# Performance work log

Measured on AMD Instinct MI355X. Metric: run time of the kernel, lower is better.

Reference implementation:

```python
import jax, jax.numpy as jnp
import numpy as np

# dims per module source / chosen globals
B, LB = 4, 28            # new frames, buffered frames; M = B+LB = L = 32
DK, DV = 256, 32         # Dk=256 hardcoded; Dv = 4*len_of_lookup+4 with len_of_lookup=7
HS, WS = 64, 64          # H//8, W//8 with H=W=512
LMAX = 32                # memory cap L
TRAIN_SZ = 1000          # log base train_sz
ALPHA = 0.5              # blend coefficient (original inits 0, which zeroes the branch)
# log(L*h*w + h*w, train_sz) / sqrt(Dk)
SCALE = float(np.log(LMAX * HS * WS + HS * WS) / np.log(TRAIN_SZ) / np.sqrt(DK))


def _xavier(key, fan_in, fan_out):
    lim = np.sqrt(6.0 / (fan_in + fan_out))
    return jax.random.uniform(key, (fan_in, fan_out), jnp.float32, -lim, lim)


def setup_inputs() -> dict:
    key = jax.random.key(0)
    ks = jax.random.split(key, 7)
    return {
        "fc": jax.random.normal(ks[0], (B, DK, HS, WS), jnp.float32),
        "fm": jax.random.normal(ks[1], (B, DV, HS, WS), jnp.float32),
        "key_buffer": jax.random.normal(ks[2], (LB, DK, HS, WS), jnp.float32),
        "value_buffer": jax.random.normal(ks[3], (LB, DV, HS, WS), jnp.float32),
        "Q": _xavier(ks[4], DK, DK),
        "K": _xavier(ks[5], DK, DK),
        "V": _xavier(ks[6], DV, DV),
    }


def reference(fc, fm, key_buffer, value_buffer, Q, K, V):
    # matmul = einsum('ijkl,jm->imkl'): per-pixel channel mixing
    q = jnp.einsum('bdhw,de->behw', fc, Q)                      # [B,Dk,h,w]
    k = jnp.concatenate([jnp.einsum('bdhw,de->behw', fc, K), key_buffer], axis=0)    # [M,Dk,h,w]
    v = jnp.concatenate([jnp.einsum('bdhw,de->behw', fm, V), value_buffer], axis=0)  # [M,Dv,h,w]
    # current_batch (=1) < L, so no slicing of k/v on this step
    scores = SCALE * jnp.einsum('bdhw,mdhw->bmhw', q, k)        # [B,M,h,w]
    attn = jax.nn.softmax(scores, axis=-1)                      # NOTE: softmax over width axis, as in source (dim=-1)
    ctx = jnp.einsum('bmhw,mdhw->bdhw', attn, v)                # [B,Dv,h,w]
    return fm + ALPHA * ctx
```

## Files before the change

kernel.cpp:

```cpp
#include <hip/hip_runtime.h>
#include <hip/hip_bf16.h>
#include <cmath>

#define NB 4
#define NM 32
#define DKc 256
#define DVc 32
#define NP 4096

using bf16x8 = __attribute__((ext_vector_type(8))) short;
using f32x4  = __attribute__((ext_vector_type(4))) float;

__device__ __forceinline__ unsigned short f2bf(float f) {
    union { float f; unsigned u; } x; x.f = f;
    unsigned r = 0x7FFFu + ((x.u >> 16) & 1u);
    return (unsigned short)((x.u + r) >> 16);
}

__global__ __launch_bounds__(256) void k_prep(
    const float* __restrict__ fc, unsigned short* __restrict__ fcT,
    const float* __restrict__ Q, unsigned short* __restrict__ WTq,
    const float* __restrict__ K, unsigned short* __restrict__ WTk,
    const float* __restrict__ fm, const float* __restrict__ V, float* __restrict__ vproj) {
    int x = blockIdx.x;
    int t = threadIdx.x;
    if (x < 1056) {
        __shared__ float tile[64][65];
        const float* s; unsigned short* d; int R, C, r0, c0;
        if (x < 1024) {
            int bb = x >> 8, rest = x & 255;
            R = 256; C = 4096;
            r0 = (rest >> 6) * 64; c0 = (rest & 63) * 64;
            s = fc + (long)bb * 256 * 4096; d = fcT + (long)bb * 256 * 4096;
        } else {
            int i = x - 1024;
            int mat = i >> 4, idx = i & 15;
            R = 256; C = 256;
            r0 = (idx >> 2) * 64; c0 = (idx & 3) * 64;
            s = mat ? K : Q; d = mat ? WTk : WTq;
        }
        #pragma unroll
        for (int j = 0; j < 16; ++j) {
            int i = t + 256 * j;
            int r = i >> 6, c = i & 63;
            tile[r][c] = s[(long)(r0 + r) * C + c0 + c];
        }
        __syncthreads();
        #pragma unroll
        for (int j = 0; j < 8; ++j) {
            int i = t + 256 * j;
            int row = i >> 5;
            int pr = i & 31;
            float f0 = tile[2 * pr][row];
            float f1 = tile[2 * pr + 1][row];
            unsigned pack = (unsigned)f2bf(f0) | ((unsigned)f2bf(f1) << 16);
            reinterpret_cast<unsigned*>(d)[(((long)(c0 + row) * R + r0) >> 1) + pr] = pack;
        }
    } else {
        __shared__ float Vl[32][32];
        __shared__ float fml[32][256];
        int i = x - 1056;
        int b = i >> 4, p0 = (i & 15) * 256;
        #pragma unroll
        for (int j = 0; j < 4; ++j) { int ii = t + 256 * j; Vl[ii >> 5][ii & 31] = V[ii]; }
        for (int j = 0; j < 32; ++j) {
            int ii = t + 256 * j;
            int dd = ii >> 8, c = ii & 255;
            fml[dd][c] = fm[((long)b * DVc + dd) * NP + p0 + c];
        }
        __syncthreads();
        float acc[32];
        #pragma unroll
        for (int e = 0; e < 32; ++e) acc[e] = 0.f;
        for (int dd = 0; dd < 32; ++dd) {
            float fv = fml[dd][t];
            #pragma unroll
            for (int e = 0; e < 32; ++e) acc[e] += fv * Vl[dd][e];
        }
        #pragma unroll
        for (int e = 0; e < 32; ++e) vproj[((long)b * DVc + e) * NP + p0 + t] = acc[e];
    }
}

__global__ __launch_bounds__(256) void k_proj(
    const unsigned short* __restrict__ WTq, const unsigned short* __restrict__ WTk,
    const unsigned short* __restrict__ fcT,
    float* __restrict__ qproj, float* __restrict__ kproj) {
    int t = threadIdx.x;
    int wave = t >> 6, lane = t & 63;
    int y = blockIdx.y;
    int b = y & 3, mat = y >> 2;
    int p0 = blockIdx.x * 64;
    int ln = lane & 15, quad = lane >> 4;
    const unsigned short* WT = mat ? WTk : WTq;
    float* dst = mat ? kproj : qproj;
    int e0w = wave * 64;
    const unsigned short* bbase = fcT + ((long)b * NP + p0 + ln) * DKc + quad * 8;
    f32x4 acc[4][4] = {};
    for (int kk = 0; kk < DKc; kk += 32) {
        bf16x8 a[4], bb[4];
        #pragma unroll
        for (int i = 0; i < 4; ++i)
            a[i] = *reinterpret_cast<const bf16x8*>(WT + (long)(e0w + i * 16 + ln) * DKc + quad * 8 + kk);
        #pragma unroll
        for (int j = 0; j < 4; ++j)
            bb[j] = *reinterpret_cast<const bf16x8*>(bbase + (long)j * 16 * DKc + kk);
        #pragma unroll
        for (int i = 0; i < 4; ++i)
            #pragma unroll
            for (int j = 0; j < 4; ++j)
                acc[i][j] = __builtin_amdgcn_mfma_f32_16x16x32_bf16(a[i], bb[j], acc[i][j], 0, 0, 0);
    }
    #pragma unroll
    for (int i = 0; i < 4; ++i)
        #pragma unroll
        for (int j = 0; j < 4; ++j)
            #pragma unroll
            for (int r = 0; r < 4; ++r) {
                int e = e0w + i * 16 + quad * 4 + r, p = p0 + j * 16 + ln;
                dst[((long)b * DKc + e) * NP + p] = acc[i][j][r];
            }
}

__global__ __launch_bounds__(256, 2) void k_scores(
    const float* __restrict__ qproj, const float* __restrict__ kproj,
    const float* __restrict__ kbuf, float* __restrict__ partial) {
    int t = threadIdx.x;
    int wseg = blockIdx.x, ec = blockIdx.y, b = blockIdx.z;
    int w = wseg * 256 + t;
    int e0 = ec * 32;
    const float* qp = qproj + ((long)b * DKc + e0) * NP + w;
    float acc[NM];
    #pragma unroll
    for (int m = 0; m < NM; ++m) acc[m] = 0.f;
    #pragma unroll 2
    for (int e = 0; e < 32; ++e) {
        float qv = qp[(long)e * NP];
        float kv[NM];
        #pragma unroll
        for (int m = 0; m < NM; ++m) {
            const float* kp = (m < 4 ? kproj + (long)m * DKc * NP
                                     : kbuf + (long)(m - 4) * DKc * NP);
            kv[m] = kp[(long)(e0 + e) * NP + w];
        }
        #pragma unroll
        for (int m = 0; m < NM; ++m) acc[m] += qv * kv[m];
    }
    float* pp = partial + (((long)b * 8 + ec) * NM) * NP + w;
    #pragma unroll
    for (int m = 0; m < NM; ++m) pp[(long)m * NP] = acc[m];
}

__global__ __launch_bounds__(512) void k_out(
    const float* __restrict__ partial, const float* __restrict__ vproj,
    const float* __restrict__ vbuf, const float* __restrict__ fm,
    float* __restrict__ out, float scale) {
    __shared__ float sc[32][68];
    int t = threadIdx.x;
    int b = blockIdx.x >> 6, hrow = blockIdx.x & 63;
    int p0h = hrow * 64;
    int wave = t >> 6, lane = t & 63;
    {
        int w = t & 63, mg = t >> 6;
        float s[4] = {0.f, 0.f, 0.f, 0.f};
        #pragma unroll
        for (int c = 0; c < 8; ++c) {
            const float* pp = partial + (((long)b * 8 + c) * NM + mg * 4) * NP + p0h + w;
            #pragma unroll
            for (int mi = 0; mi < 4; ++mi) s[mi] += pp[(long)mi * NP];
        }
        #pragma unroll
        for (int mi = 0; mi < 4; ++mi) sc[mg * 4 + mi][w] = s[mi] * scale;
    }
    __syncthreads();
    #pragma unroll
    for (int r = 0; r < 4; ++r) {
        int m = wave * 4 + r;
        float x = sc[m][lane];
        float mx = x;
        #pragma unroll
        for (int d = 1; d < 64; d <<= 1) mx = fmaxf(mx, __shfl_xor(mx, d));
        float e = __expf(x - mx);
        float sum = e;
        #pragma unroll
        for (int d = 1; d < 64; d <<= 1) sum += __shfl_xor(sum, d);
        sc[m][lane] = e / sum;
    }
    __syncthreads();
    {
        int dg = t >> 6, w = t & 63;
        float c4[4] = {0.f, 0.f, 0.f, 0.f};
        #pragma unroll
        for (int m = 0; m < NM; ++m) {
            float a = sc[m][w];
            const float* vp = (m < 4 ? vproj + (long)m * DVc * NP : vbuf + (long)(m - 4) * DVc * NP)
                              + (long)(dg * 4) * NP + p0h + w;
            #pragma unroll
            for (int i = 0; i < 4; ++i) c4[i] += a * vp[(long)i * NP];
        }
        #pragma unroll
        for (int i = 0; i < 4; ++i) {
            long gi = ((long)b * DVc + dg * 4 + i) * NP + p0h + w;
            out[gi] = fm[gi] + 0.5f * c4[i];
        }
    }
}

extern "C" void kernel_launch(void* const* d_in, const int* in_sizes, int n_in,
                              void* d_out, int out_size, void* d_ws, size_t ws_size,
                              hipStream_t stream) {
    const float* fc = (const float*)d_in[0];
    const float* fm = (const float*)d_in[1];
    const float* kb = (const float*)d_in[2];
    const float* vb = (const float*)d_in[3];
    const float* Q  = (const float*)d_in[4];
    const float* K  = (const float*)d_in[5];
    const float* V  = (const float*)d_in[6];
    float* out = (float*)d_out;
    char* ws = (char*)d_ws;
    float*          qproj = (float*)(ws);
    float*          kproj = (float*)(ws + 16777216);
    float*          vproj = (float*)(ws + 33554432);
    unsigned short* fcT   = (unsigned short*)(ws + 35651584);
    unsigned short* WTq   = (unsigned short*)(ws + 44040192);
    unsigned short* WTk   = (unsigned short*)(ws + 44171264);
    float*          partial = (float*)(ws + 35651584);
    float scale = (float)(log(135168.0) / log(1000.0) / 16.0);

    hipLaunchKernelGGL(k_prep, dim3(1120), dim3(256), 0, stream,
                       fc, fcT, Q, WTq, K, WTk, fm, V, vproj);
    hipLaunchKernelGGL(k_proj, dim3(64, 8), dim3(256), 0, stream,
                       WTq, WTk, fcT, qproj, kproj);
    hipLaunchKernelGGL(k_scores, dim3(16, 8, 4), dim3(256), 0, stream,
                       qproj, kproj, kb, partial);
    hipLaunchKernelGGL(k_out, dim3(256), dim3(512), 0, stream,
                       partial, vproj, vb, fm, out, scale);
}
```

Before: 266.9 us.

## Retile score kernel over batch and key groups to reuse key loads

The score kernel is reorganised so each block computes all four query batches against a group of four memory keys, instead of one batch against all 32 keys. Each key slice is now read from global memory once rather than once per batch, while query slices are re-read once per key group. Loads and stores also move to two-wide float vectors per thread. The grid changes to 8x8x8 blocks. The trade-off is more query traffic and a different register footprint per thread.

```diff
diff --git a/kernel.cpp b/kernel.cpp
--- a/kernel.cpp
+++ b/kernel.cpp
@@ -10,6 +10,7 @@
 
 using bf16x8 = __attribute__((ext_vector_type(8))) short;
 using f32x4  = __attribute__((ext_vector_type(4))) float;
+using f32x2  = __attribute__((ext_vector_type(2))) float;
 
 __device__ __forceinline__ unsigned short f2bf(float f) {
     union { float f; unsigned u; } x; x.f = f;
@@ -126,29 +127,54 @@
     const float* __restrict__ qproj, const float* __restrict__ kproj,
     const float* __restrict__ kbuf, float* __restrict__ partial) {
     int t = threadIdx.x;
-    int wseg = blockIdx.x, ec = blockIdx.y, b = blockIdx.z;
-    int w = wseg * 256 + t;
+    int wseg = blockIdx.x, ec = blockIdx.y, mq = blockIdx.z;
+    int w0 = wseg * 512 + t * 2;
     int e0 = ec * 32;
-    const float* qp = qproj + ((long)b * DKc + e0) * NP + w;
-    float acc[NM];
-    #pragma unroll
-    for (int m = 0; m < NM; ++m) acc[m] = 0.f;
-    #pragma unroll 2
-    for (int e = 0; e < 32; ++e) {
-        float qv = qp[(long)e * NP];
-        float kv[NM];
-        #pragma unroll
-        for (int m = 0; m < NM; ++m) {
-            const float* kp = (m < 4 ? kproj + (long)m * DKc * NP
-                                     : kbuf + (long)(m - 4) * DKc * NP);
-            kv[m] = kp[(long)(e0 + e) * NP + w];
-        }
-        #pragma unroll
-        for (int m = 0; m < NM; ++m) acc[m] += qv * kv[m];
-    }
-    float* pp = partial + (((long)b * 8 + ec) * NM) * NP + w;
-    #pragma unroll
-    for (int m = 0; m < NM; ++m) pp[(long)m * NP] = acc[m];
+    const float* kp[4];
+    #pragma unroll
+    for (int mi = 0; mi < 4; ++mi) {
+        int m = mq * 4 + mi;
+        kp[mi] = (m < 4 ? kproj + (long)m * DKc * NP : kbuf + (long)(m - 4) * DKc * NP)
+                 + (long)e0 * NP + w0;
+    }
+    const float* qp[4];
+    #pragma unroll
+    for (int b = 0; b < 4; ++b)
+        qp[b] = qproj + ((long)b * DKc + e0) * NP + w0;
+
+    f32x2 acc[4][4];
+    #pragma unroll
+    for (int b = 0; b < 4; ++b)
+        #pragma unroll
+        for (int mi = 0; mi < 4; ++mi) acc[b][mi] = (f32x2){0.f, 0.f};
+
+    for (int e4 = 0; e4 < 32; e4 += 4) {
+        f32x2 qv[4][4], kv[4][4];
+        #pragma unroll
+        for (int u = 0; u < 4; ++u) {
+            long off = (long)(e4 + u) * NP;
+            #pragma unroll
+            for (int b = 0; b < 4; ++b)
+                qv[u][b] = *reinterpret_cast<const f32x2*>(qp[b] + off);
+            #pragma unroll
+            for (int mi = 0; mi < 4; ++mi)
+                kv[u][mi] = *reinterpret_cast<const f32x2*>(kp[mi] + off);
+        }
+        #pragma unroll
+        for (int u = 0; u < 4; ++u)
+            #pragma unroll
+            for (int b = 0; b < 4; ++b)
+                #pragma unroll
+                for (int mi = 0; mi < 4; ++mi)
+                    acc[b][mi] += qv[u][b] * kv[u][mi];
+    }
+    #pragma unroll
+    for (int b = 0; b < 4; ++b)
+        #pragma unroll
+        for (int mi = 0; mi < 4; ++mi) {
+            float* pp = partial + (((long)b * 8 + ec) * NM + mq * 4 + mi) * NP + w0;
+            *reinterpret_cast<f32x2*>(pp) = acc[b][mi];
+        }
 }
 
 __global__ __launch_bounds__(512) void k_out(
@@ -231,7 +257,7 @@
                        fc, fcT, Q, WTq, K, WTk, fm, V, vproj);
     hipLaunchKernelGGL(k_proj, dim3(64, 8), dim3(256), 0, stream,
                        WTq, WTk, fcT, qproj, kproj);
-    hipLaunchKernelGGL(k_scores, dim3(16, 8, 4), dim3(256), 0, stream,
+    hipLaunchKernelGGL(k_scores, dim3(8, 8, 8), dim3(256), 0, stream,
                        qproj, kproj, kb, partial);
     hipLaunchKernelGGL(k_out, dim3(256), dim3(512), 0, stream,
                        partial, vproj, vb, fm, out, scale);
```

Result: faster. 244.8 us (-8.3%).
